# Kernel optimization log

Measured on AMD Instinct MI355X. Metric: run time of the kernel, lower is better.

Reference implementation:

```python
import jax, jax.numpy as jnp
import numpy as np

DIM = 512
HID = 2048
EPS = 1e-5


def setup_inputs() -> dict:
    key = jax.random.key(0)
    ks = jax.random.split(key, 11)
    B, S = 256, 100
    def lin(kw, fan_in, fan_out):
        # torch Linear init: U(-1/sqrt(fan_in), 1/sqrt(fan_in)); stored as [in, out]
        bound = 1.0 / np.sqrt(fan_in)
        return jax.random.uniform(kw, (fan_in, fan_out), jnp.float32, -bound, bound)
    def bias(kb, fan_in, fan_out):
        bound = 1.0 / np.sqrt(fan_in)
        return jax.random.uniform(kb, (fan_out,), jnp.float32, -bound, bound)
    return {
        "x": jax.random.normal(ks[0], (B, S, DIM), jnp.float32),
        "W_w": lin(ks[1], DIM, HID),  "W_b": bias(ks[2], DIM, HID),
        "WK_w": lin(ks[3], HID, HID), "WK_b": bias(ks[4], HID, HID),
        "WQ_w": lin(ks[5], HID, HID), "WQ_b": bias(ks[6], HID, HID),
        "WV_w": lin(ks[7], HID, HID), "WV_b": bias(ks[8], HID, HID),
        "W2_w": lin(ks[9], HID, DIM), "W2_b": bias(ks[10], HID, DIM),
    }


def reference(x, W_w, W_b, WK_w, WK_b, WQ_w, WQ_b, WV_w, WV_b, W2_w, W2_b):
    S = x.shape[1]
    # torch: tril(ones, diagonal=1) -> token i may attend to j <= i+1
    mask = jnp.tril(jnp.ones((S, S), dtype=bool), k=1)
    residual = x
    h = jax.nn.relu(x @ W_w + W_b)            # [B,S,HID]
    K = h @ WK_w + WK_b
    Q = h @ WQ_w + WQ_b
    V = h @ WV_w + WV_b
    # note: original scales by sqrt(dim)=sqrt(512), not sqrt(hidden_dim)
    attn = jnp.einsum('bqh,bkh->bqk', Q, K) / np.sqrt(DIM)
    attn = jnp.where(mask, attn, -jnp.inf)
    attn = jax.nn.softmax(attn, axis=-1)
    o = jnp.einsum('bqk,bkh->bqh', attn, V)
    y = o @ W2_w + W2_b + residual            # [B,S,DIM]
    # F.layer_norm over x.shape[1:] == (S, DIM), no affine
    mu = jnp.mean(y, axis=(1, 2), keepdims=True)
    var = jnp.var(y, axis=(1, 2), keepdims=True)
    return (y - mu) * jax.lax.rsqrt(var + EPS)
```

## Files before the change

kernel.cpp:

```cpp
#include <hip/hip_runtime.h>
#include <hip/hip_bf16.h>

typedef unsigned int u32;
typedef unsigned short u16;
typedef __attribute__((ext_vector_type(4))) float f32x4;
typedef __attribute__((ext_vector_type(8))) short s16x8;
typedef __attribute__((ext_vector_type(4))) u16 u16x4;
typedef __attribute__((ext_vector_type(8))) u16 u16x8;

#define DEVFN __device__ __forceinline__

DEVFN u16 f2bf(float f) {
  u32 x = __builtin_bit_cast(u32, f);
  u32 r = x + 0x7fffu + ((x >> 16) & 1u);
  return (u16)(r >> 16);
}

DEVFN float bf2f(u16 b) { return __builtin_bit_cast(float, (u32)b << 16); }

DEVFN void gload_lds16(const u16* g, u16* l) {
  __builtin_amdgcn_global_load_lds((const __attribute__((address_space(1))) u32*)g,
                                   (__attribute__((address_space(3))) u32*)l, 16, 0, 0);
}

#define KQV_PHASE(Q, VMWAIT, DOSTAGE)                                          \
  {                                                                            \
    if (DOSTAGE) {                                                             \
      const int g_ = (Q) + 2;                                                  \
      const int sl_ = (g_ & 3) * 8192;                                         \
      const int k0_ = (g_ >> 1) * 64 + (g_ & 1) * 32;                          \
      gload_lds16(aS0 + k0_, smemw + sl_ + ldst);                              \
      gload_lds16(aS1 + k0_, smemw + sl_ + 4096 + ldst);                       \
      gload_lds16(bS0 + k0_, smemw + 32768 + sl_ + ldst);                      \
      gload_lds16(bS1 + k0_, smemw + 32768 + sl_ + 4096 + ldst);               \
    }                                                                          \
    VMWAIT;                                                                    \
    __builtin_amdgcn_s_barrier();                                              \
    {                                                                          \
      const int sl_ = (Q) & 3;                                                 \
      const u16* As_ = smem + sl_ * 8192;                                      \
      const u16* Bs_ = smem + 32768 + sl_ * 8192;                              \
      s16x8 fa_[8], fb_[4];                                                    \
      _Pragma("unroll") for (int mf = 0; mf < 8; ++mf)                         \
          fa_[mf] = *(const s16x8*)(As_ + baseA + mf * 512);                   \
      _Pragma("unroll") for (int nf = 0; nf < 4; ++nf)                         \
          fb_[nf] = *(const s16x8*)(Bs_ + baseB + nf * 512);                   \
      __builtin_amdgcn_s_setprio(1);                                           \
      _Pragma("unroll") for (int mf = 0; mf < 8; ++mf)                         \
        _Pragma("unroll") for (int nf = 0; nf < 4; ++nf)                       \
          acc[mf][nf] = __builtin_amdgcn_mfma_f32_16x16x32_bf16(               \
              fa_[mf], fb_[nf], acc[mf][nf], 0, 0, 0);                         \
      __builtin_amdgcn_s_setprio(0);                                           \
    }                                                                          \
    __builtin_amdgcn_sched_barrier(0);                                         \
  }

#define WAITV4 asm volatile("s_waitcnt vmcnt(4)" ::: "memory")
#define WAITV0 asm volatile("s_waitcnt vmcnt(0)" ::: "memory")
#define WAITNONE ((void)0)

template<int RELU>
__launch_bounds__(512, 2)
__global__ void gemm256(const u16* __restrict__ Ag, int lda,
                        const u16* __restrict__ Bg, int ldb,
                        u16* __restrict__ C, int ldc,
                        const float* __restrict__ bias,
                        int M, int K, int ntiles) {
  extern __shared__ u16 smem_dyn[];
  const u16* smem = smem_dyn;
  u16* smemw = smem_dyn;

  const int tid = threadIdx.x;
  const int lane = tid & 63, wave = tid >> 6;
  const int wm = wave >> 2, wn = wave & 3;
  const int l15 = lane & 15, l4 = lane >> 4;

  const int nwg = gridDim.x;
  const int q8 = nwg >> 3, r8 = nwg & 7;
  const int xcd = blockIdx.x & 7, io = blockIdx.x >> 3;
  const int wg = (xcd < r8) ? (xcd * (q8 + 1) + io)
                            : (r8 * (q8 + 1) + (xcd - r8) * q8 + io);
  const int m0 = (wg / ntiles) * 256, n0 = (wg % ntiles) * 256;

  const int chunkSwz = (l4 ^ ((l15 >> 1) & 3)) * 8;
  const int baseA = (wm * 128 + l15) * 32 + chunkSwz;
  const int baseB = (wn * 64 + l15) * 32 + chunkSwz;

  const int srow = tid >> 2;
  const int scol = (((tid & 3) ^ ((tid >> 3) & 3))) * 8;
  long ar0 = m0 + srow;        if (ar0 > M - 1) ar0 = M - 1;
  long ar1 = m0 + 128 + srow;  if (ar1 > M - 1) ar1 = M - 1;
  const u16* aS0 = Ag + ar0 * (long)lda + scol;
  const u16* aS1 = Ag + ar1 * (long)lda + scol;
  const u16* bS0 = Bg + (long)(n0 + srow) * ldb + scol;
  const u16* bS1 = Bg + (long)(n0 + 128 + srow) * ldb + scol;
  const int ldst = tid * 8;

  f32x4 acc[8][4];
#pragma unroll
  for (int i = 0; i < 8; ++i)
#pragma unroll
    for (int j = 0; j < 4; ++j) acc[i][j] = (f32x4){0.f, 0.f, 0.f, 0.f};

  const int NT = K >> 6;

  {
#pragma unroll
    for (int g_ = 0; g_ < 2; ++g_) {
      const int k0_ = g_ * 32;
      gload_lds16(aS0 + k0_, smemw + g_ * 8192 + ldst);
      gload_lds16(aS1 + k0_, smemw + g_ * 8192 + 4096 + ldst);
      gload_lds16(bS0 + k0_, smemw + 32768 + g_ * 8192 + ldst);
      gload_lds16(bS1 + k0_, smemw + 32768 + g_ * 8192 + 4096 + ldst);
    }
    __builtin_amdgcn_sched_barrier(0);
  }

  for (int t = 0; t < NT - 1; ++t) {
    KQV_PHASE(2 * t,     WAITV4, true);
    KQV_PHASE(2 * t + 1, WAITV4, true);
  }
  KQV_PHASE(2 * NT - 2, WAITV0,   false);
  KQV_PHASE(2 * NT - 1, WAITNONE, false);

#pragma unroll
  for (int mf = 0; mf < 8; ++mf) {
#pragma unroll
    for (int nf = 0; nf < 4; ++nf) {
      const int n = n0 + wn * 64 + nf * 16 + l15;
      const float bv = bias[n];
#pragma unroll
      for (int r = 0; r < 4; ++r) {
        const int s = wm * 128 + mf * 16 + l4 * 4 + r;
        if (m0 + s >= M) continue;
        float v = acc[mf][nf][r] + bv;
        if (RELU) v = v > 0.f ? v : 0.f;
        C[(long)(m0 + s) * ldc + n] = f2bf(v);
      }
    }
  }
}

template<int MODE>
__launch_bounds__(256)
__global__ void gemm_bt(const u16* __restrict__ Ag, int lda, int aRPB, int aRowMax,
                        const u16* __restrict__ Bg, int ldb, int bRPB, int bRowMax,
                        void* __restrict__ Cptr, int ldc, int cRPB, int cRowGuard,
                        const float* __restrict__ bias, const float* __restrict__ resid,
                        int K, float scale) {
  __shared__ __align__(16) u16 As[128 * 64];
  __shared__ __align__(16) u16 Bs[128 * 64];
  const int tid = threadIdx.x;
  const int lane = tid & 63, wid = tid >> 6;
  const int l15 = lane & 15, l4 = lane >> 4;
  const int wr = wid >> 1, wc = wid & 1;
  const int m0 = blockIdx.x * 128, n0 = blockIdx.y * 128;
  int b = blockIdx.z;
  long koff = 0;
  if (MODE == 5) { koff = (long)(b & 3) * K; b >>= 2; }

  const u16* aSrc[4];
  const u16* bSrc[4];
  u16* aDst[4];
  u16* bDst[4];
#pragma unroll
  for (int i = 0; i < 4; ++i) {
    int c = i * 256 + tid;
    int r = c >> 3, g = c & 7;
    long arow = (long)b * aRPB + m0 + r; if (arow > aRowMax) arow = aRowMax;
    aSrc[i] = Ag + arow * (long)lda + koff + g * 8;
    aDst[i] = &As[c * 8];
    long brow = (long)b * bRPB + n0 + r; if (brow > bRowMax) brow = bRowMax;
    bSrc[i] = Bg + brow * (long)ldb + koff + g * 8;
    bDst[i] = &Bs[c * 8];
  }

  f32x4 acc[4][4];
#pragma unroll
  for (int i = 0; i < 4; ++i)
#pragma unroll
    for (int j = 0; j < 4; ++j) acc[i][j] = (f32x4){0.f, 0.f, 0.f, 0.f};

  for (int kt = 0; kt < K; kt += 64) {
#pragma unroll
    for (int i = 0; i < 4; ++i) gload_lds16(aSrc[i] + kt, aDst[i]);
#pragma unroll
    for (int i = 0; i < 4; ++i) gload_lds16(bSrc[i] + kt, bDst[i]);
    __syncthreads();
#pragma unroll
    for (int kk = 0; kk < 2; ++kk) {
      s16x8 af[4], bfr[4];
#pragma unroll
      for (int mi = 0; mi < 4; ++mi) {
        int rr = wr * 64 + mi * 16 + l15;
        af[mi] = *(const s16x8*)&As[rr * 64 + kk * 32 + l4 * 8];
      }
#pragma unroll
      for (int ni = 0; ni < 4; ++ni) {
        int rr = wc * 64 + ni * 16 + l15;
        bfr[ni] = *(const s16x8*)&Bs[rr * 64 + kk * 32 + l4 * 8];
      }
#pragma unroll
      for (int mi = 0; mi < 4; ++mi)
#pragma unroll
        for (int ni = 0; ni < 4; ++ni)
          acc[mi][ni] = __builtin_amdgcn_mfma_f32_16x16x32_bf16(af[mi], bfr[ni], acc[mi][ni], 0, 0, 0);
    }
    __syncthreads();
  }

  const long cRow0 = (long)b * cRPB + m0;
#pragma unroll
  for (int mi = 0; mi < 4; ++mi) {
#pragma unroll
    for (int ni = 0; ni < 4; ++ni) {
      const int n = n0 + wc * 64 + ni * 16 + l15;
      float bv = 0.f;
      if (MODE == 4) bv = bias[n];
#pragma unroll
      for (int r = 0; r < 4; ++r) {
        const int s = wr * 64 + mi * 16 + l4 * 4 + r;
        if (m0 + s >= cRowGuard) continue;
        const long ci = (cRow0 + s) * (long)ldc + n;
        float v = acc[mi][ni][r];
        if (MODE == 3)      { ((u16*)Cptr)[ci] = f2bf(v); }
        else if (MODE == 5) { atomicAdd((float*)Cptr + ci, v * scale); }
        else                { ((float*)Cptr)[ci] = v + bv + resid[ci]; }
      }
    }
  }
}

__launch_bounds__(256)
__global__ void softmax_rows(const float* __restrict__ S, const float* __restrict__ vv,
                             u16* __restrict__ P, float sc) {
  const int wid = threadIdx.x >> 6, lane = threadIdx.x & 63;
  const long rowg = (long)blockIdx.x * 4 + wid;
  const int i = (int)(rowg & 127);
  const int b = (int)(rowg >> 7);
  const float* srow = S + rowg * 128;
  const float* vvb = vv + b * 100;
  u16* prow = P + rowg * 128;
  if (i >= 100) { prow[lane] = 0; prow[lane + 64] = 0; return; }
  const int jmax = (i + 1 < 99) ? i + 1 : 99;
  bool v0 = lane <= jmax, v1 = (lane + 64) <= jmax;
  float s0 = v0 ? srow[lane] + vvb[lane] * sc : -3e38f;
  float s1 = v1 ? srow[lane + 64] + vvb[lane + 64] * sc : -3e38f;
  float m = fmaxf(s0, s1);
#pragma unroll
  for (int off = 32; off; off >>= 1) m = fmaxf(m, __shfl_xor(m, off));
  float e0 = v0 ? __expf(s0 - m) : 0.f;
  float e1 = v1 ? __expf(s1 - m) : 0.f;
  float sum = e0 + e1;
#pragma unroll
  for (int off = 32; off; off >>= 1) sum += __shfl_xor(sum, off);
  float rs = 1.f / sum;
  prow[lane] = f2bf(e0 * rs);
  prow[lane + 64] = f2bf(e1 * rs);
}

__launch_bounds__(256)
__global__ void transpose_cast_w(const float* __restrict__ W, u16* __restrict__ Wt,
                                 int K, int N) {
  __shared__ __align__(16) float t[64][68];
  const int tid = threadIdx.x;
  const int n0 = blockIdx.x * 64, k0 = blockIdx.y * 64;
#pragma unroll
  for (int it = 0; it < 4; ++it) {
    int c = it * 256 + tid;
    int r = c >> 4, cc = (c & 15) * 4;
    f32x4 v = *(const f32x4*)&W[(long)(k0 + r) * N + n0 + cc];
    *(f32x4*)&t[r][cc] = v;
  }
  __syncthreads();
#pragma unroll
  for (int it = 0; it < 4; ++it) {
    int c = it * 256 + tid;
    int n = c >> 4, kk = (c & 15) * 4;
    u16x4 o;
#pragma unroll
    for (int j = 0; j < 4; ++j) o[j] = f2bf(t[kk + j][n]);
    *(u16x4*)&Wt[(long)(n0 + n) * K + k0 + kk] = o;
  }
}

__launch_bounds__(256)
__global__ void cast_f32_to_bf16(const float* __restrict__ in, u16* __restrict__ out, long n4) {
  for (long i = (long)blockIdx.x * 256 + threadIdx.x; i < n4; i += (long)gridDim.x * 256) {
    f32x4 v = *(const f32x4*)&in[i * 4];
    u16x4 o;
#pragma unroll
    for (int j = 0; j < 4; ++j) o[j] = f2bf(v[j]);
    *(u16x4*)&out[i * 4] = o;
  }
}

__launch_bounds__(256)
__global__ void rowdot_f32(const float* __restrict__ M, const float* __restrict__ v,
                           float* __restrict__ o, int ncols) {
  __shared__ float red[4];
  const float* r = M + (long)blockIdx.x * ncols;
  const int tid = threadIdx.x;
  float s = 0.f;
  for (int d = tid; d < ncols; d += 256) s += r[d] * v[d];
#pragma unroll
  for (int off = 32; off; off >>= 1) s += __shfl_down(s, off);
  if ((tid & 63) == 0) red[tid >> 6] = s;
  __syncthreads();
  if (tid == 0) o[blockIdx.x] = red[0] + red[1] + red[2] + red[3];
}

__launch_bounds__(256)
__global__ void vv_dot(const u16* __restrict__ H, const float* __restrict__ w,
                       float* __restrict__ o) {
  __shared__ float red[4];
  const u16* r = H + (long)blockIdx.x * 2048;
  const int tid = threadIdx.x;
  u16x8 hv = *(const u16x8*)&r[tid * 8];
  float s = 0.f;
#pragma unroll
  for (int j = 0; j < 8; ++j) s += bf2f(hv[j]) * w[tid * 8 + j];
#pragma unroll
  for (int off = 32; off; off >>= 1) s += __shfl_down(s, off);
  if ((tid & 63) == 0) red[tid >> 6] = s;
  __syncthreads();
  if (tid == 0) o[blockIdx.x] = red[0] + red[1] + red[2] + red[3];
}

__launch_bounds__(256)
__global__ void bias_w2(const float* __restrict__ bV, const float* __restrict__ W2w,
                        float* __restrict__ o) {
  int n = blockIdx.x * 256 + threadIdx.x;
  float s = 0.f;
  for (int h = 0; h < 2048; ++h) s += bV[h] * W2w[h * 512 + n];
  o[n] = s;
}

__launch_bounds__(256)
__global__ void transpose_vt(const u16* __restrict__ V, u16* __restrict__ Vt,
                             int vstride, int nH) {
  __shared__ __align__(16) u16 t[64][72];
  const int tid = threadIdx.x;
  const int h0 = blockIdx.x * 64, s0 = blockIdx.y * 64, b = blockIdx.z;
#pragma unroll
  for (int it = 0; it < 2; ++it) {
    int c = it * 256 + tid;
    int s = c >> 3, hh = (c & 7) * 8;
    u16x8 v = {0, 0, 0, 0, 0, 0, 0, 0};
    if (s0 + s < 100) v = *(const u16x8*)&V[((long)b * 100 + s0 + s) * vstride + h0 + hh];
    *(u16x8*)&t[s][hh] = v;
  }
  __syncthreads();
#pragma unroll
  for (int it = 0; it < 2; ++it) {
    int c = it * 256 + tid;
    int h = c >> 3, ss = (c & 7) * 8;
    u16x8 o;
#pragma unroll
    for (int j = 0; j < 8; ++j) o[j] = t[ss + j][h];
    *(u16x8*)&Vt[((long)b * nH + h0 + h) * 128 + s0 + ss] = o;
  }
}

__launch_bounds__(256)
__global__ void ln_stats(const float* __restrict__ y, float* __restrict__ stats) {
  __shared__ float rs[256], rq[256];
  const int b = blockIdx.x, tid = threadIdx.x;
  const float* yb = y + (long)b * 51200;
  float s = 0.f, q = 0.f;
  for (int i = tid; i < 51200; i += 256) { float v = yb[i]; s += v; q += v * v; }
  rs[tid] = s; rq[tid] = q;
  __syncthreads();
  for (int off = 128; off; off >>= 1) {
    if (tid < off) { rs[tid] += rs[tid + off]; rq[tid] += rq[tid + off]; }
    __syncthreads();
  }
  if (tid == 0) {
    float mean = rs[0] * (1.f / 51200.f);
    float var = rq[0] * (1.f / 51200.f) - mean * mean;
    stats[b * 2] = mean;
    stats[b * 2 + 1] = rsqrtf(var + 1e-5f);
  }
}

__launch_bounds__(256)
__global__ void ln_apply(float* __restrict__ y, const float* __restrict__ stats) {
  const long i4 = (long)blockIdx.x * 256 + threadIdx.x;
  const int b = (int)(i4 / 12800);
  float mu = stats[b * 2], rstd = stats[b * 2 + 1];
  f32x4 v = *(const f32x4*)&y[i4 * 4];
#pragma unroll
  for (int j = 0; j < 4; ++j) v[j] = (v[j] - mu) * rstd;
  *(f32x4*)&y[i4 * 4] = v;
}

extern "C" void kernel_launch(void* const* d_in, const int* in_sizes, int n_in,
                              void* d_out, int out_size, void* d_ws, size_t ws_size,
                              hipStream_t stream) {
  const float* x    = (const float*)d_in[0];
  const float* W_w  = (const float*)d_in[1];
  const float* W_b  = (const float*)d_in[2];
  const float* WK_w = (const float*)d_in[3];
  const float* WK_b = (const float*)d_in[4];
  const float* WQ_w = (const float*)d_in[5];
  const float* WQ_b = (const float*)d_in[6];
  const float* WV_w = (const float*)d_in[7];
  const float* WV_b = (const float*)d_in[8];
  const float* W2_w = (const float*)d_in[9];
  const float* W2_b = (const float*)d_in[10];
  float* out = (float*)d_out;
  const float SC = 0.044194173824159216f;

  const size_t FIXED = 26214400ull + 2097152ull + 10485760ull + 2097152ull +
                       3ull * 8388608ull + 10240ull + 8192ull + 2048ull + 262144ull;
  const size_t PERB = 1151376ull;
  int CH = 256;
  if (ws_size == 0) CH = 32;
  else { while (CH > 4 && FIXED + (size_t)CH * PERB + 4096 > ws_size) CH >>= 1; }
  const int NCH = 256 / CH;
  const int CHR = CH * 100;
  const int MT256 = (CHR + 255) / 256;

  char* p = (char*)d_ws;
  auto carve = [&](size_t bytes) { char* r = p; p += (bytes + 255) & ~(size_t)255; return r; };
  u16* xb     = (u16*)carve(26214400);
  u16* W1t    = (u16*)carve(2097152);
  u16* WTt    = (u16*)carve(10485760);
  u16* W2t    = (u16*)carve(2097152);
  u16* WVb    = (u16*)carve(8388608);
  u16* WKb    = (u16*)carve(8388608);
  u16* WQb    = (u16*)carve(8388608);
  float* bias2 = (float*)carve(10240);
  float* wv   = (float*)carve(8192);
  float* stats = (float*)carve(2048);
  u16* h    = (u16*)carve((size_t)CH * 409600);
  u16* TW   = (u16*)carve((size_t)CH * 512000);
  float* sc = (float*)carve((size_t)CH * 65536);
  u16* P    = (u16*)carve((size_t)CH * 32768);
  u16* VW2T = (u16*)carve((size_t)CH * 131072);
  float* vv = (float*)carve((size_t)CH * 400);

  cast_f32_to_bf16<<<2048, 256, 0, stream>>>(x, xb, 3276800);
  cast_f32_to_bf16<<<1024, 256, 0, stream>>>(WV_w, WVb, 1048576);
  cast_f32_to_bf16<<<1024, 256, 0, stream>>>(WK_w, WKb, 1048576);
  cast_f32_to_bf16<<<1024, 256, 0, stream>>>(WQ_w, WQb, 1048576);
  transpose_cast_w<<<dim3(32, 8), 256, 0, stream>>>(W_w,  W1t, 512, 2048);
  transpose_cast_w<<<dim3(8, 32), 256, 0, stream>>>(W2_w, W2t, 2048, 512);
  gemm_bt<3><<<dim3(16, 16, 1), 256, 0, stream>>>(WKb, 2048, 0, 2047, WQb, 2048, 0, 2047,
                                                  WTt, 2048, 0, 1 << 30,
                                                  nullptr, nullptr, 2048, 1.f);
  gemm_bt<3><<<dim3(4, 16, 1), 256, 0, stream>>>(W2t, 2048, 0, 511, WVb, 2048, 0, 2047,
                                                 WTt + (size_t)2048 * 2048, 2048, 0, 1 << 30,
                                                 nullptr, nullptr, 2048, 1.f);
  rowdot_f32<<<2048, 256, 0, stream>>>(WK_w, WQ_b, wv, 2048);
  hipMemsetAsync(bias2, 0, 2560 * 4, stream);
  bias_w2<<<2, 256, 0, stream>>>(WV_b, W2_w, bias2 + 2048);

  for (int c = 0; c < NCH; ++c) {
    const u16* xc = xb + (size_t)c * CHR * 512;
    const float* xf = x + (size_t)c * CHR * 512;
    float* outc = out + (size_t)c * CHR * 512;

    gemm256<1><<<MT256 * 8, 512, 131072, stream>>>(xc, 512, W1t, 512,
                                                   h, 2048, W_b, CHR, 512, 8);
    gemm256<0><<<MT256 * 10, 512, 131072, stream>>>(h, 2048, WTt, 2048,
                                                    TW, 2560, bias2, CHR, 2048, 10);
    vv_dot<<<CHR, 256, 0, stream>>>(h, wv, vv);
    hipMemsetAsync(sc, 0, (size_t)CH * 65536, stream);
    gemm_bt<5><<<dim3(1, 1, CH * 4), 256, 0, stream>>>(TW, 2560, 100, CHR - 1,
                                                       h, 2048, 100, CHR - 1,
                                                       sc, 128, 128, 1 << 30, nullptr, nullptr,
                                                       512, SC);
    softmax_rows<<<CH * 32, 256, 0, stream>>>(sc, vv, P, SC);
    transpose_vt<<<dim3(8, 2, CH), 256, 0, stream>>>(TW + 2048, VW2T, 2560, 512);
    gemm_bt<4><<<dim3(1, 4, CH), 256, 0, stream>>>(P, 128, 128, CH * 128 - 1,
                                                   VW2T, 128, 512, CH * 512 - 1,
                                                   outc, 512, 100, 100, W2_b, xf, 128, 1.f);
  }

  ln_stats<<<256, 256, 0, stream>>>(out, stats);
  ln_apply<<<12800, 256, 0, stream>>>(out, stats);
}
```

Baseline: 942.0 us.

## Fuse layernorm stats into output GEMM and replace split-K atomics with slices

The output GEMM epilogue now reduces per-block sums and sums of squares into a partials buffer, which removes the separate ln_stats pass that re-read the whole output. The split-K score GEMM writes four separate slices instead of using atomicAdd into a zeroed buffer, so the memset goes away and softmax sums the slices when it loads them. The bf16 weight copies are now overlaid on the per-chunk workspace to make room for the larger score buffer. In exchange the score buffer is four times larger and softmax reads more data.

```diff
diff --git a/kernel.cpp b/kernel.cpp
--- a/kernel.cpp
+++ b/kernel.cpp
@@ -147,7 +147,8 @@
                         const u16* __restrict__ Bg, int ldb, int bRPB, int bRowMax,
                         void* __restrict__ Cptr, int ldc, int cRPB, int cRowGuard,
                         const float* __restrict__ bias, const float* __restrict__ resid,
-                        int K, float scale) {
+                        int K, float scale, float* __restrict__ part, int pbase,
+                        long sliceE) {
   __shared__ __align__(16) u16 As[128 * 64];
   __shared__ __align__(16) u16 Bs[128 * 64];
   const int tid = threadIdx.x;
@@ -156,8 +157,9 @@
   const int wr = wid >> 1, wc = wid & 1;
   const int m0 = blockIdx.x * 128, n0 = blockIdx.y * 128;
   int b = blockIdx.z;
+  int zslice = 0;
   long koff = 0;
-  if (MODE == 5) { koff = (long)(b & 3) * K; b >>= 2; }
+  if (MODE == 6) { zslice = b & 3; koff = (long)zslice * K; b >>= 2; }
 
   const u16* aSrc[4];
   const u16* bSrc[4];
@@ -210,6 +212,7 @@
   }
 
   const long cRow0 = (long)b * cRPB + m0;
+  float lsum = 0.f, lsq = 0.f;
 #pragma unroll
   for (int mi = 0; mi < 4; ++mi) {
 #pragma unroll
@@ -220,20 +223,37 @@
 #pragma unroll
       for (int r = 0; r < 4; ++r) {
         const int s = wr * 64 + mi * 16 + l4 * 4 + r;
-        if (m0 + s >= cRowGuard) continue;
-        const long ci = (cRow0 + s) * (long)ldc + n;
-        float v = acc[mi][ni][r];
-        if (MODE == 3)      { ((u16*)Cptr)[ci] = f2bf(v); }
-        else if (MODE == 5) { atomicAdd((float*)Cptr + ci, v * scale); }
-        else                { ((float*)Cptr)[ci] = v + bv + resid[ci]; }
+        if (m0 + s < cRowGuard) {
+          const long ci = (cRow0 + s) * (long)ldc + n;
+          float v = acc[mi][ni][r];
+          if (MODE == 3)      { ((u16*)Cptr)[ci] = f2bf(v); }
+          else if (MODE == 6) { ((float*)Cptr)[(long)zslice * sliceE + ci] = v * scale; }
+          else                { v += bv + resid[ci]; ((float*)Cptr)[ci] = v;
+                                lsum += v; lsq += v * v; }
+        }
       }
     }
   }
+
+  if (MODE == 4) {
+    float* shs = (float*)As;
+    float* shq = (float*)Bs;
+    shs[tid] = lsum; shq[tid] = lsq;
+    __syncthreads();
+    for (int off = 128; off; off >>= 1) {
+      if (tid < off) { shs[tid] += shs[tid + off]; shq[tid] += shq[tid + off]; }
+      __syncthreads();
+    }
+    if (tid == 0) {
+      part[((long)pbase + b) * 8 + blockIdx.y * 2]     = shs[0];
+      part[((long)pbase + b) * 8 + blockIdx.y * 2 + 1] = shq[0];
+    }
+  }
 }
 
 __launch_bounds__(256)
 __global__ void softmax_rows(const float* __restrict__ S, const float* __restrict__ vv,
-                             u16* __restrict__ P, float sc) {
+                             u16* __restrict__ P, float sc, long sliceE) {
   const int wid = threadIdx.x >> 6, lane = threadIdx.x & 63;
   const long rowg = (long)blockIdx.x * 4 + wid;
   const int i = (int)(rowg & 127);
@@ -244,8 +264,12 @@
   if (i >= 100) { prow[lane] = 0; prow[lane + 64] = 0; return; }
   const int jmax = (i + 1 < 99) ? i + 1 : 99;
   bool v0 = lane <= jmax, v1 = (lane + 64) <= jmax;
-  float s0 = v0 ? srow[lane] + vvb[lane] * sc : -3e38f;
-  float s1 = v1 ? srow[lane + 64] + vvb[lane + 64] * sc : -3e38f;
+  float a0 = srow[lane]            + srow[sliceE + lane] +
+             srow[2 * sliceE + lane] + srow[3 * sliceE + lane];
+  float a1 = srow[lane + 64]            + srow[sliceE + lane + 64] +
+             srow[2 * sliceE + lane + 64] + srow[3 * sliceE + lane + 64];
+  float s0 = v0 ? a0 + vvb[lane] * sc : -3e38f;
+  float s1 = v1 ? a1 + vvb[lane + 64] * sc : -3e38f;
   float m = fmaxf(s0, s1);
 #pragma unroll
   for (int off = 32; off; off >>= 1) m = fmaxf(m, __shfl_xor(m, off));
@@ -363,34 +387,18 @@
 }
 
 __launch_bounds__(256)
-__global__ void ln_stats(const float* __restrict__ y, float* __restrict__ stats) {
-  __shared__ float rs[256], rq[256];
-  const int b = blockIdx.x, tid = threadIdx.x;
-  const float* yb = y + (long)b * 51200;
-  float s = 0.f, q = 0.f;
-  for (int i = tid; i < 51200; i += 256) { float v = yb[i]; s += v; q += v * v; }
-  rs[tid] = s; rq[tid] = q;
-  __syncthreads();
-  for (int off = 128; off; off >>= 1) {
-    if (tid < off) { rs[tid] += rs[tid + off]; rq[tid] += rq[tid + off]; }
-    __syncthreads();
-  }
-  if (tid == 0) {
-    float mean = rs[0] * (1.f / 51200.f);
-    float var = rq[0] * (1.f / 51200.f) - mean * mean;
-    stats[b * 2] = mean;
-    stats[b * 2 + 1] = rsqrtf(var + 1e-5f);
-  }
-}
-
-__launch_bounds__(256)
-__global__ void ln_apply(float* __restrict__ y, const float* __restrict__ stats) {
+__global__ void ln_apply(float* __restrict__ y, const float* __restrict__ part) {
   const long i4 = (long)blockIdx.x * 256 + threadIdx.x;
   const int b = (int)(i4 / 12800);
-  float mu = stats[b * 2], rstd = stats[b * 2 + 1];
+  const float* pb = part + (long)b * 8;
+  const float s = pb[0] + pb[2] + pb[4] + pb[6];
+  const float q = pb[1] + pb[3] + pb[5] + pb[7];
+  const float mean = s * (1.f / 51200.f);
+  const float var = q * (1.f / 51200.f) - mean * mean;
+  const float rstd = rsqrtf(var + 1e-5f);
   f32x4 v = *(const f32x4*)&y[i4 * 4];
 #pragma unroll
-  for (int j = 0; j < 4; ++j) v[j] = (v[j] - mu) * rstd;
+  for (int j = 0; j < 4; ++j) v[j] = (v[j] - mean) * rstd;
   *(f32x4*)&y[i4 * 4] = v;
 }
 
@@ -412,14 +420,23 @@
   const float SC = 0.044194173824159216f;
 
   const size_t FIXED = 26214400ull + 2097152ull + 10485760ull + 2097152ull +
-                       3ull * 8388608ull + 10240ull + 8192ull + 2048ull + 262144ull;
-  const size_t PERB = 1151376ull;
+                       10240ull + 8192ull + 8192ull + 262144ull;
+  const size_t PERB = 1348224ull;
+  const size_t PREPOVL = 25165824ull + 65536ull;
   int CH = 256;
   if (ws_size == 0) CH = 32;
-  else { while (CH > 4 && FIXED + (size_t)CH * PERB + 4096 > ws_size) CH >>= 1; }
+  else {
+    while (CH > 4) {
+      size_t chunkBytes = (size_t)CH * PERB;
+      if (chunkBytes < PREPOVL) chunkBytes = PREPOVL;
+      if (FIXED + chunkBytes + 4096 <= ws_size) break;
+      CH >>= 1;
+    }
+  }
   const int NCH = 256 / CH;
   const int CHR = CH * 100;
   const int MT256 = (CHR + 255) / 256;
+  const long SLICE = (long)CH * 16384;
 
   char* p = (char*)d_ws;
   auto carve = [&](size_t bytes) { char* r = p; p += (bytes + 255) & ~(size_t)255; return r; };
@@ -427,18 +444,19 @@
   u16* W1t    = (u16*)carve(2097152);
   u16* WTt    = (u16*)carve(10485760);
   u16* W2t    = (u16*)carve(2097152);
-  u16* WVb    = (u16*)carve(8388608);
-  u16* WKb    = (u16*)carve(8388608);
-  u16* WQb    = (u16*)carve(8388608);
   float* bias2 = (float*)carve(10240);
   float* wv   = (float*)carve(8192);
-  float* stats = (float*)carve(2048);
+  float* part = (float*)carve(8192);
+  char* chunk0 = p;
   u16* h    = (u16*)carve((size_t)CH * 409600);
   u16* TW   = (u16*)carve((size_t)CH * 512000);
-  float* sc = (float*)carve((size_t)CH * 65536);
+  float* sc = (float*)carve((size_t)CH * 262144);
   u16* P    = (u16*)carve((size_t)CH * 32768);
   u16* VW2T = (u16*)carve((size_t)CH * 131072);
   float* vv = (float*)carve((size_t)CH * 400);
+  u16* WVb = (u16*)chunk0;
+  u16* WKb = WVb + 2048 * 2048;
+  u16* WQb = WKb + 2048 * 2048;
 
   cast_f32_to_bf16<<<2048, 256, 0, stream>>>(x, xb, 3276800);
   cast_f32_to_bf16<<<1024, 256, 0, stream>>>(WV_w, WVb, 1048576);
@@ -448,10 +466,12 @@
   transpose_cast_w<<<dim3(8, 32), 256, 0, stream>>>(W2_w, W2t, 2048, 512);
   gemm_bt<3><<<dim3(16, 16, 1), 256, 0, stream>>>(WKb, 2048, 0, 2047, WQb, 2048, 0, 2047,
                                                   WTt, 2048, 0, 1 << 30,
-                                                  nullptr, nullptr, 2048, 1.f);
+                                                  nullptr, nullptr, 2048, 1.f,
+                                                  nullptr, 0, 0);
   gemm_bt<3><<<dim3(4, 16, 1), 256, 0, stream>>>(W2t, 2048, 0, 511, WVb, 2048, 0, 2047,
                                                  WTt + (size_t)2048 * 2048, 2048, 0, 1 << 30,
-                                                 nullptr, nullptr, 2048, 1.f);
+                                                 nullptr, nullptr, 2048, 1.f,
+                                                 nullptr, 0, 0);
   rowdot_f32<<<2048, 256, 0, stream>>>(WK_w, WQ_b, wv, 2048);
   hipMemsetAsync(bias2, 0, 2560 * 4, stream);
   bias_w2<<<2, 256, 0, stream>>>(WV_b, W2_w, bias2 + 2048);
@@ -466,18 +486,17 @@
     gemm256<0><<<MT256 * 10, 512, 131072, stream>>>(h, 2048, WTt, 2048,
                                                     TW, 2560, bias2, CHR, 2048, 10);
     vv_dot<<<CHR, 256, 0, stream>>>(h, wv, vv);
-    hipMemsetAsync(sc, 0, (size_t)CH * 65536, stream);
-    gemm_bt<5><<<dim3(1, 1, CH * 4), 256, 0, stream>>>(TW, 2560, 100, CHR - 1,
+    gemm_bt<6><<<dim3(1, 1, CH * 4), 256, 0, stream>>>(TW, 2560, 100, CHR - 1,
                                                        h, 2048, 100, CHR - 1,
                                                        sc, 128, 128, 1 << 30, nullptr, nullptr,
-                                                       512, SC);
-    softmax_rows<<<CH * 32, 256, 0, stream>>>(sc, vv, P, SC);
+                                                       512, SC, nullptr, 0, SLICE);
+    softmax_rows<<<CH * 32, 256, 0, stream>>>(sc, vv, P, SC, SLICE);
     transpose_vt<<<dim3(8, 2, CH), 256, 0, stream>>>(TW + 2048, VW2T, 2560, 512);
     gemm_bt<4><<<dim3(1, 4, CH), 256, 0, stream>>>(P, 128, 128, CH * 128 - 1,
                                                    VW2T, 128, 512, CH * 512 - 1,
-                                                   outc, 512, 100, 100, W2_b, xf, 128, 1.f);
-  }
-
-  ln_stats<<<256, 256, 0, stream>>>(out, stats);
-  ln_apply<<<12800, 256, 0, stream>>>(out, stats);
-}
+                                                   outc, 512, 100, 100, W2_b, xf, 128, 1.f,
+                                                   part, c * CH, 0);
+  }
+
+  ln_apply<<<12800, 256, 0, stream>>>(out, part);
+}
```

After: 807.7 us. 14.3% less time.
